# Performance work log

Measured on AMD Instinct MI355X. Metric: run time of the kernel, lower is better.

## Reference

```python
import jax, jax.numpy as jnp
import numpy as np

DIM = 512   # feature channels (dim)
K = 3       # depthwise kernel size
H = 256     # grid extent along pos[:,0]
W = 256     # grid extent along pos[:,1]
N = 20000   # number of occupied spots (unique coordinates)


def setup_inputs() -> dict:
    key = jax.random.key(0)
    k1, k2, k3 = jax.random.split(key, 3)
    rng = np.random.default_rng(0)
    # N unique flat cells; pin corners so the dense grid extent is exactly HxW
    flat = np.concatenate([[0, H * W - 1], rng.permutation(H * W - 2)[: N - 2] + 1])
    pos = jnp.asarray(np.stack([flat // W, flat % W], axis=1), dtype=jnp.int32)  # (N,2)
    x = jax.random.normal(k1, (1, N, DIM), jnp.float32)
    weight = jax.random.normal(k2, (DIM, 1, K, K), jnp.float32) * 0.05  # depthwise OIHW
    bias = jax.random.normal(k3, (DIM,), jnp.float32) * 0.05
    return {"x": x, "pos": pos, "weight": weight, "bias": bias}


def reference(x, pos, weight, bias):
    pos = pos - pos.min(axis=0)                 # shift to origin (as torch)
    p0, p1 = pos[:, 0], pos[:, 1]
    xsq = x[0]                                  # (N, DIM)
    # scatter sparse coords to dense grid (duplicates would sum, coords unique)
    grid = jnp.zeros((H, W, DIM), x.dtype).at[p0, p1].add(xsq)   # (H, W, DIM)
    xd = grid.transpose(2, 1, 0)[None]          # (1, DIM, W, H) == permute(2,1,0).unsqueeze(0)
    conv = jax.lax.conv_general_dilated(
        xd, weight, (1, 1), "SAME",
        dimension_numbers=("NCHW", "OIHW", "NCHW"),
        feature_group_count=DIM,
    ) + bias[None, :, None, None]
    mask = xd.sum(axis=1, keepdims=True) != 0.0  # occupied cells
    out_d = jnp.where(mask, conv, 0.0) + xd      # masked residual
    dense = out_d[0].transpose(2, 1, 0)          # (H, W, DIM)
    # gather back to sparse values; torch to_sparse(2) orders rows lexicographically
    order = jnp.lexsort((p1, p0))
    vals = dense[p0[order], p1[order]]           # (N, DIM)
    return vals[None]                            # (1, N, DIM)
```

## Files before the change

kernel.cpp:

```cpp
#include <hip/hip_runtime.h>

#define HH 256
#define WW 256
#define DIM 512

typedef float f32x4 __attribute__((ext_vector_type(4)));


__global__ __launch_bounds__(256) void scatter_kernel(const int* __restrict__ pos,
                                                      int* __restrict__ cell_map,
                                                      int n) {
    int i = blockIdx.x * 256 + threadIdx.x;
    if (i >= n) return;
    int p0 = pos[2 * i];
    int p1 = pos[2 * i + 1];
    cell_map[p0 * WW + p1] = i;
}

__global__ __launch_bounds__(256) void rank_kernel(const int* __restrict__ cell_map,
                                                   int* __restrict__ sorted) {
    __shared__ int red[256];
    __shared__ int wt[4];
    const int t = threadIdx.x;
    const int b = blockIdx.x;
    const int limit = b * 256;

    int cnt = 0;
    const int4* cm4 = (const int4*)cell_map;
    for (int i = t; i * 4 < limit; i += 256) {
        int4 v = cm4[i];
        cnt += (v.x >= 0) + (v.y >= 0) + (v.z >= 0) + (v.w >= 0);
    }
    red[t] = cnt;
    __syncthreads();
    #pragma unroll
    for (int d = 128; d > 0; d >>= 1) {
        if (t < d) red[t] += red[t + d];
        __syncthreads();
    }
    int blk_off = red[0];

    int cell = limit + t;
    int m = cell_map[cell];
    bool occ = (m >= 0);
    unsigned long long mask = __ballot(occ);
    int lane = t & 63;
    int wave = t >> 6;
    int pre = __popcll(mask & ((1ull << lane) - 1ull));
    if (lane == 0) wt[wave] = __popcll(mask);
    __syncthreads();
    int woff = 0;
    for (int i = 0; i < wave; ++i) woff += wt[i];
    if (occ) sorted[blk_off + woff + pre] = (m << 16) | cell;
}

__global__ __launch_bounds__(256) void conv_main(const float* __restrict__ x,
                                                 const float* __restrict__ weight,
                                                 const float* __restrict__ bias,
                                                 const int* __restrict__ cell_map,
                                                 const int* __restrict__ sorted,
                                                 float* __restrict__ out,
                                                 int n) {
    const int lane = threadIdx.x & 63;
    const int wv   = threadIdx.x >> 6;
    const int c0   = lane * 8;

    float wtv[72];
    {
        const float4* wb = (const float4*)(weight + c0 * 9);
        #pragma unroll
        for (int q = 0; q < 18; ++q) {
            float4 v = wb[q];
            wtv[4 * q + 0] = v.x; wtv[4 * q + 1] = v.y;
            wtv[4 * q + 2] = v.z; wtv[4 * q + 3] = v.w;
        }
    }
    float bj[8];
    {
        float4 b0 = *(const float4*)(bias + c0);
        float4 b1 = *(const float4*)(bias + c0 + 4);
        bj[0]=b0.x; bj[1]=b0.y; bj[2]=b0.z; bj[3]=b0.w;
        bj[4]=b1.x; bj[5]=b1.y; bj[6]=b1.z; bj[7]=b1.w;
    }
    #pragma unroll
    for (int j = 0; j < 8; ++j) wtv[j * 9 + 4] += 1.0f;

    const int nb  = gridDim.x;
    const int cid = (blockIdx.x & 7) * (nb >> 3) + (blockIdx.x >> 3);
    const int ppb = (n + nb - 1) / nb;
    const int base = cid * ppb;
    int endr = base + ppb; if (endr > n) endr = n;

    int r = base + wv;
    if (r >= endr) return;
    int pk = __builtin_amdgcn_readfirstlane(sorted[r]);

    while (r < endr) {
        const int rn = r + 4;
        int pk_next = 0;
        if (rn < endr)
            pk_next = __builtin_amdgcn_readfirstlane(sorted[rn]);

        const int p    = pk >> 16;
        const int flat = pk & 0xFFFF;
        const int h = flat >> 8;
        const int w = flat & (WW - 1);

        int m[9];
        #pragma unroll
        for (int k = 0; k < 9; ++k) {
            if (k == 4) { m[4] = -1; continue; }
            int dh = k % 3 - 1;
            int dw = k / 3 - 1;
            int hh = h + dh;
            int ww = w + dw;
            int v = -1;
            if ((unsigned)hh < (unsigned)HH && (unsigned)ww < (unsigned)WW)
                v = cell_map[hh * WW + ww];
            m[k] = __builtin_amdgcn_readfirstlane(v);
        }

        const float* xs = x + (size_t)p * DIM + c0;
        float4 s0 = *(const float4*)(xs);
        float4 s1 = *(const float4*)(xs + 4);
        float acc[8];
        acc[0] = bj[0] + s0.x * wtv[0*9+4]; acc[1] = bj[1] + s0.y * wtv[1*9+4];
        acc[2] = bj[2] + s0.z * wtv[2*9+4]; acc[3] = bj[3] + s0.w * wtv[3*9+4];
        acc[4] = bj[4] + s1.x * wtv[4*9+4]; acc[5] = bj[5] + s1.y * wtv[5*9+4];
        acc[6] = bj[6] + s1.z * wtv[6*9+4]; acc[7] = bj[7] + s1.w * wtv[7*9+4];

        #pragma unroll
        for (int k = 0; k < 9; ++k) {
            if (k == 4) continue;
            if (m[k] >= 0) {
                const float* xn = x + (size_t)m[k] * DIM + c0;
                float4 n0 = *(const float4*)(xn);
                float4 n1 = *(const float4*)(xn + 4);
                acc[0] += n0.x * wtv[0*9+k]; acc[1] += n0.y * wtv[1*9+k];
                acc[2] += n0.z * wtv[2*9+k]; acc[3] += n0.w * wtv[3*9+k];
                acc[4] += n1.x * wtv[4*9+k]; acc[5] += n1.y * wtv[5*9+k];
                acc[6] += n1.z * wtv[6*9+k]; acc[7] += n1.w * wtv[7*9+k];
            }
        }

        float* op = out + (size_t)r * DIM + c0;
        f32x4 o0 = { acc[0], acc[1], acc[2], acc[3] };
        f32x4 o1 = { acc[4], acc[5], acc[6], acc[7] };
        __builtin_nontemporal_store(o0, (f32x4*)op);
        __builtin_nontemporal_store(o1, (f32x4*)(op + 4));

        r = rn;
        pk = pk_next;
    }
}

extern "C" void kernel_launch(void* const* d_in, const int* in_sizes, int n_in,
                              void* d_out, int out_size, void* d_ws, size_t ws_size,
                              hipStream_t stream) {
    const float* x      = (const float*)d_in[0];
    const int*   pos    = (const int*)d_in[1];
    const float* weight = (const float*)d_in[2];
    const float* bias   = (const float*)d_in[3];
    float* out = (float*)d_out;

    int n = in_sizes[1] / 2;

    int* ws       = (int*)d_ws;
    int* cell_map = ws;
    int* sorted   = ws + HH * WW;

    scatter_kernel<<<(n + 255) / 256, 256, 0, stream>>>(pos, cell_map, n);
    rank_kernel<<<256, 256, 0, stream>>>(cell_map, sorted);

    const int nblocks = 1024;
    conv_main<<<nblocks, 256, 0, stream>>>(x, weight, bias, cell_map, sorted, out, n);
}
```

Baseline: 128.5 us.

## Precompute per-row neighbor index table in rank kernel for conv gather

The rank kernel now writes a 16-int row per occupied cell holding its source index and the eight neighbor indices, instead of a single packed source and cell word. The conv kernel reads this table with three int4 loads per row, prefetched one iteration ahead, rather than doing eight dependent cell_map lookups and readfirstlane calls. This is meant to shorten the index-lookup latency chain inside the main loop, at the cost of extra writes and scattered cell_map reads in the rank kernel. The conv grid also shrinks from 1024 to 768 blocks. Neighbor indices now come from an int4 vector load rather than readfirstlane, so they may not be treated as wave-uniform scalars.

```diff
diff --git a/kernel.cpp b/kernel.cpp
--- a/kernel.cpp
+++ b/kernel.cpp
@@ -18,7 +18,7 @@
 }
 
 __global__ __launch_bounds__(256) void rank_kernel(const int* __restrict__ cell_map,
-                                                   int* __restrict__ sorted) {
+                                                   int* __restrict__ nbr) {
     __shared__ int red[256];
     __shared__ int wt[4];
     const int t = threadIdx.x;
@@ -51,18 +51,36 @@
     __syncthreads();
     int woff = 0;
     for (int i = 0; i < wave; ++i) woff += wt[i];
-    if (occ) sorted[blk_off + woff + pre] = (m << 16) | cell;
+
+    if (occ) {
+        int rk = blk_off + woff + pre;
+        int h = cell >> 8;
+        int w = cell & (WW - 1);
+        int* row = nbr + rk * 16;
+        row[0] = m;
+        #pragma unroll
+        for (int k = 0; k < 9; ++k) {
+            if (k == 4) continue;
+            int dh = k % 3 - 1;
+            int dw = k / 3 - 1;
+            int hh = h + dh;
+            int ww = w + dw;
+            int v = -1;
+            if ((unsigned)hh < (unsigned)HH && (unsigned)ww < (unsigned)WW)
+                v = cell_map[hh * WW + ww];
+            row[(k < 4 ? k : k - 1) + 1] = v;
+        }
+    }
 }
 
 __global__ __launch_bounds__(256) void conv_main(const float* __restrict__ x,
                                                  const float* __restrict__ weight,
                                                  const float* __restrict__ bias,
-                                                 const int* __restrict__ cell_map,
-                                                 const int* __restrict__ sorted,
+                                                 const int* __restrict__ nbr,
                                                  float* __restrict__ out,
                                                  int n) {
     const int lane = threadIdx.x & 63;
-    const int wv   = threadIdx.x >> 6;
+    const int wv   = __builtin_amdgcn_readfirstlane(threadIdx.x >> 6);
     const int c0   = lane * 8;
 
     float wtv[72];
@@ -85,42 +103,35 @@
     #pragma unroll
     for (int j = 0; j < 8; ++j) wtv[j * 9 + 4] += 1.0f;
 
-    const int nb  = gridDim.x;
-    const int cid = (blockIdx.x & 7) * (nb >> 3) + (blockIdx.x >> 3);
-    const int ppb = (n + nb - 1) / nb;
+    const int nbk = gridDim.x;
+    const int cid = (blockIdx.x & 7) * (nbk >> 3) + (blockIdx.x >> 3);
+    const int ppb = (n + nbk - 1) / nbk;
     const int base = cid * ppb;
     int endr = base + ppb; if (endr > n) endr = n;
 
     int r = base + wv;
     if (r >= endr) return;
-    int pk = __builtin_amdgcn_readfirstlane(sorted[r]);
+
+    const int4* nb4 = (const int4*)nbr;
+    int4 A = nb4[r * 4 + 0];
+    int4 B = nb4[r * 4 + 1];
+    int4 C = nb4[r * 4 + 2];
 
     while (r < endr) {
         const int rn = r + 4;
-        int pk_next = 0;
-        if (rn < endr)
-            pk_next = __builtin_amdgcn_readfirstlane(sorted[rn]);
-
-        const int p    = pk >> 16;
-        const int flat = pk & 0xFFFF;
-        const int h = flat >> 8;
-        const int w = flat & (WW - 1);
-
-        int m[9];
-        #pragma unroll
-        for (int k = 0; k < 9; ++k) {
-            if (k == 4) { m[4] = -1; continue; }
-            int dh = k % 3 - 1;
-            int dw = k / 3 - 1;
-            int hh = h + dh;
-            int ww = w + dw;
-            int v = -1;
-            if ((unsigned)hh < (unsigned)HH && (unsigned)ww < (unsigned)WW)
-                v = cell_map[hh * WW + ww];
-            m[k] = __builtin_amdgcn_readfirstlane(v);
+        int4 An = A, Bn = B, Cn = C;
+        if (rn < endr) {
+            An = nb4[rn * 4 + 0];
+            Bn = nb4[rn * 4 + 1];
+            Cn = nb4[rn * 4 + 2];
         }
 
-        const float* xs = x + (size_t)p * DIM + c0;
+        const int ms = A.x;
+        int m[8];
+        m[0]=A.y; m[1]=A.z; m[2]=A.w; m[3]=B.x;
+        m[4]=B.y; m[5]=B.z; m[6]=B.w; m[7]=C.x;
+
+        const float* xs = x + (size_t)ms * DIM + c0;
         float4 s0 = *(const float4*)(xs);
         float4 s1 = *(const float4*)(xs + 4);
         float acc[8];
@@ -130,10 +141,10 @@
         acc[6] = bj[6] + s1.z * wtv[6*9+4]; acc[7] = bj[7] + s1.w * wtv[7*9+4];
 
         #pragma unroll
-        for (int k = 0; k < 9; ++k) {
-            if (k == 4) continue;
-            if (m[k] >= 0) {
-                const float* xn = x + (size_t)m[k] * DIM + c0;
+        for (int j = 0; j < 8; ++j) {
+            const int k = (j < 4) ? j : j + 1;
+            if (m[j] >= 0) {
+                const float* xn = x + (size_t)m[j] * DIM + c0;
                 float4 n0 = *(const float4*)(xn);
                 float4 n1 = *(const float4*)(xn + 4);
                 acc[0] += n0.x * wtv[0*9+k]; acc[1] += n0.y * wtv[1*9+k];
@@ -150,7 +161,7 @@
         __builtin_nontemporal_store(o1, (f32x4*)(op + 4));
 
         r = rn;
-        pk = pk_next;
+        A = An; B = Bn; C = Cn;
     }
 }
 
@@ -167,11 +178,11 @@
 
     int* ws       = (int*)d_ws;
     int* cell_map = ws;
-    int* sorted   = ws + HH * WW;
+    int* nbr      = ws + HH * WW;
 
     scatter_kernel<<<(n + 255) / 256, 256, 0, stream>>>(pos, cell_map, n);
-    rank_kernel<<<256, 256, 0, stream>>>(cell_map, sorted);
+    rank_kernel<<<256, 256, 0, stream>>>(cell_map, nbr);
 
-    const int nblocks = 1024;
-    conv_main<<<nblocks, 256, 0, stream>>>(x, weight, bias, cell_map, sorted, out, n);
+    const int nblocks = 768;
+    conv_main<<<nblocks, 256, 0, stream>>>(x, weight, bias, nbr, out, n);
 }
```

After: 121.9 us. 5.1% less time.
